# Kernel tuning notes

Hardware: AMD Instinct MI355X
Metric: run time of the kernel (lower is better)

Reference implementation:

```python
import jax, jax.numpy as jnp
import numpy as np

N_GENE = 50000
N_PROT = 50000
E = 500000
D = 128          # embedding_dim
C = 32           # out_channels = embedding_dim // attn_heads
F_IN = 256       # in_channels per node type
NUM_MP = 3       # metapaths: [gene-gene, gene-protein, protein-protein]


def _glorot(key, shape):
    lim = float(np.sqrt(6.0 / (shape[0] + shape[1])))
    return jax.random.uniform(key, shape, minval=-lim, maxval=lim, dtype=jnp.float32)


def setup_inputs() -> dict:
    key = jax.random.key(0)
    ks = jax.random.split(key, 24)
    inp = {
        "x_gene": jax.random.normal(ks[0], (N_GENE, F_IN), dtype=jnp.float32),
        "x_protein": jax.random.normal(ks[1], (N_PROT, F_IN), dtype=jnp.float32),
        # node-type projections linear_l / linear_r
        "Wl_gene": _glorot(ks[2], (D, F_IN)), "bl_gene": jnp.zeros((D,), jnp.float32),
        "Wr_gene": _glorot(ks[3], (D, F_IN)), "br_gene": jnp.zeros((D,), jnp.float32),
        "Wl_prot": _glorot(ks[4], (D, F_IN)), "bl_prot": jnp.zeros((D,), jnp.float32),
        "Wr_prot": _glorot(ks[5], (D, F_IN)), "br_prot": jnp.zeros((D,), jnp.float32),
        # per-metapath attention params (stacked over 3 metapaths)
        "alW": jnp.stack([_glorot(ks[6 + i], (C, D)) for i in range(NUM_MP)]),
        "alb": jnp.zeros((NUM_MP, C), jnp.float32),
        "arW": jnp.stack([_glorot(ks[9 + i], (C, D)) for i in range(NUM_MP)]),
        "arb": jnp.zeros((NUM_MP, C), jnp.float32),
        "qw": jnp.stack([_glorot(ks[12 + i], (2 * C, 1)) for i in range(NUM_MP)]),
        "sharp": jnp.ones((NUM_MP,), jnp.float32),  # 'sharpening' alpha_activation
        # per-node-type relation-weighting conv (Linear(D, 1))
        "conv_gene_W": _glorot(ks[15], (1, D)), "conv_gene_b": jnp.zeros((1,), jnp.float32),
        "conv_prot_W": _glorot(ks[16], (1, D)), "conv_prot_b": jnp.zeros((1,), jnp.float32),
        # edge indices: row 0 = head node (aggregation target), row 1 = tail node
        "edge_gg": jax.random.randint(ks[17], (2, E), 0, N_GENE, dtype=jnp.int32),
        "edge_gp": jnp.stack([jax.random.randint(ks[18], (E,), 0, N_GENE, dtype=jnp.int32),
                               jax.random.randint(ks[19], (E,), 0, N_PROT, dtype=jnp.int32)]),
        "edge_pp": jax.random.randint(ks[20], (2, E), 0, N_PROT, dtype=jnp.int32),
    }
    return inp


def _segment_softmax(scores, seg, n):
    # numerically stable softmax over variable-size neighborhoods (grouped by seg)
    m = jax.ops.segment_max(scores, seg, num_segments=n)
    m = jnp.where(jnp.isfinite(m), m, 0.0)
    ex = jnp.exp(scores - m[seg])
    denom = jax.ops.segment_sum(ex, seg, num_segments=n)
    return ex / (denom[seg] + 1e-16)


def _metapath_agg(l_head, r_tail, alW, alb, arW, arb, qw, sharp, eidx, n_head):
    # alpha_l / alpha_r node-level projections [N, C]
    al = l_head @ alW.T + alb
    ar = r_tail @ arW.T + arb
    src, dst = eidx[0], eidx[1]           # head (aggregate-at), tail (message-from)
    a_i = al[src]                          # [E, C]
    a_j = ar[dst]                          # [E, C]
    # attn_q: Tanh then Linear(2C -> 1, no bias); 'sharpening' scales the logit
    e = (jnp.tanh(jnp.concatenate([a_i, a_j], axis=1)) @ qw)[:, 0] * sharp  # [E]
    alpha = _segment_softmax(e, src, n_head)
    # message x_j * alpha, scatter-add into head nodes (aggr='add')
    return jax.ops.segment_sum(r_tail[dst] * alpha[:, None], src, num_segments=n_head)


def _relation_combine(aggs, l_self, conv_W, conv_b):
    # stack relation embeddings + self embedding: [N, R, D]
    out = jnp.stack(aggs + [l_self], axis=1)
    beta = jax.nn.softmax(out @ conv_W.T + conv_b, axis=1)  # [N, R, 1]
    return jax.nn.relu(jnp.sum(out * beta, axis=1))          # [N, D]


def reference(x_gene, x_protein, Wl_gene, bl_gene, Wr_gene, br_gene,
              Wl_prot, bl_prot, Wr_prot, br_prot,
              alW, alb, arW, arb, qw, sharp,
              conv_gene_W, conv_gene_b, conv_prot_W, conv_prot_b,
              edge_gg, edge_gp, edge_pp):
    # first layer: l/r projections from raw features
    l_gene = x_gene @ Wl_gene.T + bl_gene
    r_gene = x_gene @ Wr_gene.T + br_gene
    l_prot = x_protein @ Wl_prot.T + bl_prot
    r_prot = x_protein @ Wr_prot.T + br_prot

    # metapath 0: gene <- gene ; metapath 1: gene <- protein ; metapath 2: protein <- protein
    agg_gg = _metapath_agg(l_gene, r_gene, alW[0], alb[0], arW[0], arb[0], qw[0], sharp[0], edge_gg, N_GENE)
    agg_gp = _metapath_agg(l_gene, r_prot, alW[1], alb[1], arW[1], arb[1], qw[1], sharp[1], edge_gp, N_GENE)
    agg_pp = _metapath_agg(l_prot, r_prot, alW[2], alb[2], arW[2], arb[2], qw[2], sharp[2], edge_pp, N_PROT)

    out_gene = _relation_combine([agg_gg, agg_gp], l_gene, conv_gene_W, conv_gene_b)
    out_prot = _relation_combine([agg_pp], l_prot, conv_prot_W, conv_prot_b)
    return (out_gene, out_prot)
```

## Files before the change

kernel.cpp:

```cpp
#include <hip/hip_runtime.h>
#include <hip/hip_bf16.h>


typedef __attribute__((ext_vector_type(8))) short short8;
typedef __attribute__((ext_vector_type(4))) float floatx4;

__device__ __forceinline__ void gload16(const void* g, void* l) {
  __builtin_amdgcn_global_load_lds(
      (const __attribute__((address_space(1))) void*)g,
      (__attribute__((address_space(3))) void*)l, 16, 0, 0);
}

__device__ __forceinline__ ushort f2b(float x) {
  __hip_bfloat16 h = __float2bfloat16(x);
  return *reinterpret_cast<ushort*>(&h);
}
__device__ __forceinline__ float b2f_lo(unsigned v) { return __uint_as_float(v << 16); }
__device__ __forceinline__ float b2f_hi(unsigned v) { return __uint_as_float(v & 0xffff0000u); }

struct CvtArgs {
  const float* src[8];
  ushort* dst[8];
  int valid[8];
  int total[8];
  int bstart[9];
};
__global__ __launch_bounds__(256) void cvt_multi(CvtArgs a) {
  int b = blockIdx.x;
  int e = 0;
#pragma unroll
  for (int j = 1; j < 8; ++j)
    if (b >= a.bstart[j]) e = j;
  int i = ((b - a.bstart[e]) * 256 + threadIdx.x) * 4;
  if (i >= a.total[e]) return;
  float4 v = make_float4(0.f, 0.f, 0.f, 0.f);
  if (i < a.valid[e]) v = *(const float4*)(a.src[e] + i);
  ushort4 o;
  o.x = f2b(v.x); o.y = f2b(v.y); o.z = f2b(v.z); o.w = f2b(v.w);
  *(ushort4*)(a.dst[e] + i) = o;
}

struct ProjArgs {
  const ushort* xb[2];
  const ushort* Wb[2];
  const float* bl[2];
  const float* br[2];
  ushort* lb[2];
  ushort* rb[2];
  int N[2];
};
__global__ __launch_bounds__(256) void proj_lr_mfma(ProjArgs g) {
  const int ty = blockIdx.z;
  const ushort* xb = g.xb[ty];
  __shared__ ushort As[128 * 32];
  __shared__ ushort Bs[128 * 32];
  const int tid = threadIdx.x;
  const int lane = tid & 63;
  const int wave = tid >> 6;
  const int wm = wave & 1, wn = wave >> 1;
  const int rowBase = blockIdx.x * 128;
  const int colHalf = blockIdx.y;
  const ushort* Wbase = g.Wb[ty] + (size_t)colHalf * 128 * 256;

  floatx4 acc[4][4] = {};

  const int srow = tid >> 2, schk = tid & 3;
  for (int k0 = 0; k0 < 256; k0 += 32) {
#pragma unroll
    for (int i = 0; i < 2; ++i) {
      gload16(xb + (size_t)(rowBase + srow + i * 64) * 256 + k0 + schk * 8,
              &As[(tid + i * 256) * 8]);
      gload16(Wbase + (size_t)(srow + i * 64) * 256 + k0 + schk * 8,
              &Bs[(tid + i * 256) * 8]);
    }
    __syncthreads();
    short8 bf[4];
#pragma unroll
    for (int nt = 0; nt < 4; ++nt)
      bf[nt] = *(const short8*)&Bs[(wn * 64 + nt * 16 + (lane & 15)) * 32 + (lane >> 4) * 8];
#pragma unroll
    for (int mt = 0; mt < 4; ++mt) {
      short8 a = *(const short8*)&As[(wm * 64 + mt * 16 + (lane & 15)) * 32 + (lane >> 4) * 8];
#pragma unroll
      for (int nt = 0; nt < 4; ++nt)
        acc[mt][nt] = __builtin_amdgcn_mfma_f32_16x16x32_bf16(a, bf[nt], acc[mt][nt], 0, 0, 0);
    }
    __syncthreads();
  }

  const int N = g.N[ty];
  const float* bias = colHalf ? g.br[ty] : g.bl[ty];
  ushort* outp = colHalf ? g.rb[ty] : g.lb[ty];
#pragma unroll
  for (int mt = 0; mt < 4; ++mt)
#pragma unroll
    for (int nt = 0; nt < 4; ++nt) {
      int col = wn * 64 + nt * 16 + (lane & 15);
      float bv = bias[col];
#pragma unroll
      for (int vi = 0; vi < 4; ++vi) {
        int row = rowBase + wm * 64 + mt * 16 + (lane >> 4) * 4 + vi;
        if (row < N) outp[(size_t)row * 128 + col] = f2b(acc[mt][nt][vi] + bv);
      }
    }
}

struct AttnArgs {
  const ushort* Ab[4];
  const ushort* Wb[4];
  const float* bias[4];
  const float* q0[4];
  const float* q1[4];
  float* o0[4];
  float* o1[4];
  int N[4];
  int BN[4];
};
__global__ __launch_bounds__(256) void attn_proj_multi(AttnArgs g) {
  const int ei = blockIdx.y;
  const ushort* Ab = g.Ab[ei];
  const ushort* Wb = g.Wb[ei];
  const int N = g.N[ei], BN = g.BN[ei];
  const int NB = BN >> 4;
  __shared__ ushort As[128 * 32];
  __shared__ ushort Ws[64 * 128];
  const int tid = threadIdx.x;
  const int lane = tid & 63;
  const int wave = tid >> 6;
  const int rowBase = blockIdx.x * 128;

  for (int i = 0; i < NB; ++i) {
    int idx = tid + i * 256;
    gload16(Wb + (size_t)idx * 8, &Ws[idx * 8]);
  }

  floatx4 acc[2][4] = {};
  for (int k0 = 0; k0 < 128; k0 += 32) {
#pragma unroll
    for (int i = 0; i < 2; ++i) {
      int t = tid + i * 256;
      gload16(Ab + (size_t)(rowBase + (t >> 2)) * 128 + k0 + (t & 3) * 8, &As[t * 8]);
    }
    __syncthreads();
    short8 bf[4];
#pragma unroll
    for (int nt = 0; nt < 4; ++nt)
      if (nt < NB)
        bf[nt] = *(const short8*)&Ws[(nt * 16 + (lane & 15)) * 128 + k0 + (lane >> 4) * 8];
#pragma unroll
    for (int mt = 0; mt < 2; ++mt) {
      short8 a = *(const short8*)&As[(wave * 32 + mt * 16 + (lane & 15)) * 32 + (lane >> 4) * 8];
#pragma unroll
      for (int nt = 0; nt < 4; ++nt)
        if (nt < NB)
          acc[mt][nt] = __builtin_amdgcn_mfma_f32_16x16x32_bf16(a, bf[nt], acc[mt][nt], 0, 0, 0);
    }
    __syncthreads();
  }

  const float* bias = g.bias[ei];
  const int l15 = lane & 15;
  const bool two = (NB == 4);
  float bv[4];
#pragma unroll
  for (int nt = 0; nt < 4; ++nt) bv[nt] = (nt < NB) ? bias[nt * 16 + l15] : 0.f;
  float q0v0 = g.q0[ei][l15], q0v1 = g.q0[ei][16 + l15];
  float q1v0 = 0.f, q1v1 = 0.f;
  if (two) { q1v0 = g.q1[ei][l15]; q1v1 = g.q1[ei][16 + l15]; }
  float* o0 = g.o0[ei];
  float* o1 = g.o1[ei];
#pragma unroll
  for (int mt = 0; mt < 2; ++mt)
#pragma unroll
    for (int vi = 0; vi < 4; ++vi) {
      float slo = tanhf(acc[mt][0][vi] + bv[0]) * q0v0
                + tanhf(acc[mt][1][vi] + bv[1]) * q0v1;
      float shi = 0.f;
      if (two)
        shi = tanhf(acc[mt][2][vi] + bv[2]) * q1v0
            + tanhf(acc[mt][3][vi] + bv[3]) * q1v1;
#pragma unroll
      for (int m = 8; m >= 1; m >>= 1) {
        slo += __shfl_xor(slo, m, 64);
        shi += __shfl_xor(shi, m, 64);
      }
      const int row = rowBase + wave * 32 + mt * 16 + (lane >> 4) * 4 + vi;
      if (l15 == 0 && row < N) {
        o0[row] = slo;
        if (two) o1[row] = shi;
      }
    }
}

__global__ __launch_bounds__(256) void hist3_kernel(
    const int* __restrict__ e0, const int* __restrict__ e1,
    const int* __restrict__ e2, int* __restrict__ deg,
    int* __restrict__ rank, int E, int NG) {
  int e = blockIdx.x * 256 + threadIdx.x;
  if (e >= 3 * E) return;
  int mp = (e >= 2 * E) ? 2 : ((e >= E) ? 1 : 0);
  int el = e - mp * E;
  const int* ep = (mp == 0) ? e0 : (mp == 1) ? e1 : e2;
  int segb = (mp == 2) ? 2 * NG : mp * NG;
  rank[e] = atomicAdd(&deg[segb + ep[el]], 1);
}

__global__ __launch_bounds__(256) void scanA_kernel(
    const int* __restrict__ deg, int* __restrict__ offsets,
    int* __restrict__ tile_tot, int n) {
  __shared__ int wtot[4];
  const int t = threadIdx.x;
  const int base = blockIdx.x * 2048 + t * 8;
  int v[8], pre[8], s = 0;
#pragma unroll
  for (int j = 0; j < 8; ++j) {
    v[j] = (base + j < n) ? deg[base + j] : 0;
    pre[j] = s;
    s += v[j];
  }
  const int lane = t & 63, wv = t >> 6;
  int x = s;
#pragma unroll
  for (int o = 1; o < 64; o <<= 1) {
    int u = __shfl_up(x, o, 64);
    if (lane >= o) x += u;
  }
  if (lane == 63) wtot[wv] = x;
  __syncthreads();
  int wpre = 0;
#pragma unroll
  for (int j = 0; j < 4; ++j) wpre += (j < wv) ? wtot[j] : 0;
  int excl = wpre + x - s;
#pragma unroll
  for (int j = 0; j < 8; ++j)
    if (base + j < n) offsets[base + j] = excl + pre[j];
  if (t == 255) tile_tot[blockIdx.x] = wpre + x;
}

__global__ __launch_bounds__(256) void scanB_kernel(
    const int* __restrict__ tile_tot, int* __restrict__ tile_pre,
    int* __restrict__ offsets, int T, int n) {
  __shared__ int wtot[4];
  const int t = threadIdx.x;
  int v = (t < T) ? tile_tot[t] : 0;
  const int lane = t & 63, wv = t >> 6;
  int x = v;
#pragma unroll
  for (int o = 1; o < 64; o <<= 1) {
    int u = __shfl_up(x, o, 64);
    if (lane >= o) x += u;
  }
  if (lane == 63) wtot[wv] = x;
  __syncthreads();
  int wpre = 0;
#pragma unroll
  for (int j = 0; j < 4; ++j) wpre += (j < wv) ? wtot[j] : 0;
  if (t < T) tile_pre[t] = wpre + x - v;
  if (t == 255) offsets[n] = wpre + x;
}

__global__ __launch_bounds__(256) void scanC_kernel(
    int* __restrict__ offsets, const int* __restrict__ tile_pre, int n) {
  const int add = tile_pre[blockIdx.x];
  const int base = blockIdx.x * 2048 + threadIdx.x * 8;
#pragma unroll
  for (int j = 0; j < 8; ++j)
    if (base + j < n) offsets[base + j] += add;
}

__global__ __launch_bounds__(256) void scatter3_kernel(
    const int* __restrict__ e0, const int* __restrict__ e1,
    const int* __restrict__ e2, const int* __restrict__ rank,
    const int* __restrict__ offsets,
    const float* __restrict__ tl3, const float* __restrict__ tr3,
    const float* __restrict__ sharp, int2* __restrict__ recs,
    int E, int NG, int NP) {
  int e = blockIdx.x * 256 + threadIdx.x;
  if (e >= 3 * E) return;
  int mp = (e >= 2 * E) ? 2 : ((e >= E) ? 1 : 0);
  int el = e - mp * E;
  const int* ep = (mp == 0) ? e0 : (mp == 1) ? e1 : e2;
  int s = ep[el], d = ep[el + E];
  int hb = (mp == 2) ? 2 * NG : mp * NG;
  int tb = (mp == 0) ? 0 : (mp == 1) ? NG : NG + NP;
  float w = expf((tl3[hb + s] + tr3[tb + d]) * sharp[mp]);
  recs[offsets[hb + s] + rank[e]] = make_int2(d << 8, __float_as_int(w));
}

__global__ __launch_bounds__(256) void gather_combine(
    const ushort* __restrict__ rb_gene, const ushort* __restrict__ rb_prot,
    const ushort* __restrict__ lb_gene, const ushort* __restrict__ lb_prot,
    const int* __restrict__ offsets, const int2* __restrict__ recs,
    const float* __restrict__ cgW, const float* __restrict__ cgb,
    const float* __restrict__ cpW, const float* __restrict__ cpb,
    float* __restrict__ out_gene, float* __restrict__ out_prot,
    int NG, int NP) {
  const int lane = threadIdx.x & 63;
  const int l16 = lane & 15;
  const int node = blockIdx.x * 16 + (threadIdx.x >> 4);
  if (node >= NG + NP) return;
  const bool isGene = node < NG;
  const unsigned coloff = (unsigned)l16 << 4;
  const unsigned OMASK = 0x00FFFF00u;

  const int h0 = isGene ? node : NG + node;
  const int j0a = offsets[h0];
  const int ca = offsets[h0 + 1] - j0a;
  int j0b = 0, cb2 = 0;
  if (isGene) {
    j0b = offsets[NG + node];
    cb2 = offsets[NG + node + 1] - j0b;
  }

  float a0[8] = {0.f, 0.f, 0.f, 0.f, 0.f, 0.f, 0.f, 0.f};
  float a1[8] = {0.f, 0.f, 0.f, 0.f, 0.f, 0.f, 0.f, 0.f};
  float ds0 = 0.f, ds1 = 0.f;
  const ushort* rtA = isGene ? rb_gene : rb_prot;

  if (isGene) {
    const int cmax = (ca > cb2) ? ca : cb2;
    if (cmax > 0) {
      int2 rA0 = recs[j0a];
      int2 rA1 = recs[j0a + ((1 < ca) ? 1 : 0)];
      int2 rB0 = recs[j0b];
      int2 rB1 = recs[j0b + ((1 < cb2) ? 1 : 0)];
      const int nit = (cmax + 1) >> 1;
      for (int it = 0; it < nit; ++it) {
        const int b = it * 2;
        const float wA0 = (b < ca)      ? __int_as_float(rA0.y) : 0.f;
        const float wA1 = (b + 1 < ca)  ? __int_as_float(rA1.y) : 0.f;
        const float wB0 = (b < cb2)     ? __int_as_float(rB0.y) : 0.f;
        const float wB1 = (b + 1 < cb2) ? __int_as_float(rB1.y) : 0.f;
        const uint4 vA0 = *(const uint4*)((const char*)rtA + (((unsigned)rA0.x & OMASK) + coloff));
        const uint4 vA1 = *(const uint4*)((const char*)rtA + (((unsigned)rA1.x & OMASK) + coloff));
        const uint4 vB0 = *(const uint4*)((const char*)rb_prot + (((unsigned)rB0.x & OMASK) + coloff));
        const uint4 vB1 = *(const uint4*)((const char*)rb_prot + (((unsigned)rB1.x & OMASK) + coloff));
        const int nb = b + 2;
        rA0 = recs[j0a + ((nb < ca) ? nb : 0)];
        rA1 = recs[j0a + ((nb + 1 < ca) ? nb + 1 : 0)];
        rB0 = recs[j0b + ((nb < cb2) ? nb : 0)];
        rB1 = recs[j0b + ((nb + 1 < cb2) ? nb + 1 : 0)];
        ds0 += wA0 + wA1;
        a0[0] += b2f_lo(vA0.x) * wA0 + b2f_lo(vA1.x) * wA1;
        a0[1] += b2f_hi(vA0.x) * wA0 + b2f_hi(vA1.x) * wA1;
        a0[2] += b2f_lo(vA0.y) * wA0 + b2f_lo(vA1.y) * wA1;
        a0[3] += b2f_hi(vA0.y) * wA0 + b2f_hi(vA1.y) * wA1;
        a0[4] += b2f_lo(vA0.z) * wA0 + b2f_lo(vA1.z) * wA1;
        a0[5] += b2f_hi(vA0.z) * wA0 + b2f_hi(vA1.z) * wA1;
        a0[6] += b2f_lo(vA0.w) * wA0 + b2f_lo(vA1.w) * wA1;
        a0[7] += b2f_hi(vA0.w) * wA0 + b2f_hi(vA1.w) * wA1;
        ds1 += wB0 + wB1;
        a1[0] += b2f_lo(vB0.x) * wB0 + b2f_lo(vB1.x) * wB1;
        a1[1] += b2f_hi(vB0.x) * wB0 + b2f_hi(vB1.x) * wB1;
        a1[2] += b2f_lo(vB0.y) * wB0 + b2f_lo(vB1.y) * wB1;
        a1[3] += b2f_hi(vB0.y) * wB0 + b2f_hi(vB1.y) * wB1;
        a1[4] += b2f_lo(vB0.z) * wB0 + b2f_lo(vB1.z) * wB1;
        a1[5] += b2f_hi(vB0.z) * wB0 + b2f_hi(vB1.z) * wB1;
        a1[6] += b2f_lo(vB0.w) * wB0 + b2f_lo(vB1.w) * wB1;
        a1[7] += b2f_hi(vB0.w) * wB0 + b2f_hi(vB1.w) * wB1;
      }
    }
  } else {
    if (ca > 0) {
      int2 r0 = recs[j0a];
      int2 r1 = recs[j0a + ((1 < ca) ? 1 : 0)];
      int2 r2 = recs[j0a + ((2 < ca) ? 2 : 0)];
      int2 r3 = recs[j0a + ((3 < ca) ? 3 : 0)];
      const int nit = (ca + 3) >> 2;
      for (int it = 0; it < nit; ++it) {
        const int b = it * 4;
        const float w0 = (b < ca)     ? __int_as_float(r0.y) : 0.f;
        const float w1 = (b + 1 < ca) ? __int_as_float(r1.y) : 0.f;
        const float w2 = (b + 2 < ca) ? __int_as_float(r2.y) : 0.f;
        const float w3 = (b + 3 < ca) ? __int_as_float(r3.y) : 0.f;
        const uint4 v0 = *(const uint4*)((const char*)rtA + (((unsigned)r0.x & OMASK) + coloff));
        const uint4 v1 = *(const uint4*)((const char*)rtA + (((unsigned)r1.x & OMASK) + coloff));
        const uint4 v2 = *(const uint4*)((const char*)rtA + (((unsigned)r2.x & OMASK) + coloff));
        const uint4 v3 = *(const uint4*)((const char*)rtA + (((unsigned)r3.x & OMASK) + coloff));
        const int nb = b + 4;
        r0 = recs[j0a + ((nb < ca) ? nb : 0)];
        r1 = recs[j0a + ((nb + 1 < ca) ? nb + 1 : 0)];
        r2 = recs[j0a + ((nb + 2 < ca) ? nb + 2 : 0)];
        r3 = recs[j0a + ((nb + 3 < ca) ? nb + 3 : 0)];
        ds0 += (w0 + w1) + (w2 + w3);
        a0[0] += b2f_lo(v0.x) * w0 + b2f_lo(v1.x) * w1 + b2f_lo(v2.x) * w2 + b2f_lo(v3.x) * w3;
        a0[1] += b2f_hi(v0.x) * w0 + b2f_hi(v1.x) * w1 + b2f_hi(v2.x) * w2 + b2f_hi(v3.x) * w3;
        a0[2] += b2f_lo(v0.y) * w0 + b2f_lo(v1.y) * w1 + b2f_lo(v2.y) * w2 + b2f_lo(v3.y) * w3;
        a0[3] += b2f_hi(v0.y) * w0 + b2f_hi(v1.y) * w1 + b2f_hi(v2.y) * w2 + b2f_hi(v3.y) * w3;
        a0[4] += b2f_lo(v0.z) * w0 + b2f_lo(v1.z) * w1 + b2f_lo(v2.z) * w2 + b2f_lo(v3.z) * w3;
        a0[5] += b2f_hi(v0.z) * w0 + b2f_hi(v1.z) * w1 + b2f_hi(v2.z) * w2 + b2f_hi(v3.z) * w3;
        a0[6] += b2f_lo(v0.w) * w0 + b2f_lo(v1.w) * w1 + b2f_lo(v2.w) * w2 + b2f_lo(v3.w) * w3;
        a0[7] += b2f_hi(v0.w) * w0 + b2f_hi(v1.w) * w1 + b2f_hi(v2.w) * w2 + b2f_hi(v3.w) * w3;
      }
    }
  }

  const float inv0 = 1.f / (ds0 + 1e-16f);
  const float inv1 = 1.f / (ds1 + 1e-16f);
  float g0[8], g1[8], self[8];
#pragma unroll
  for (int c = 0; c < 8; ++c) { g0[c] = a0[c] * inv0; g1[c] = a1[c] * inv1; }
  {
    const ushort* lbp = isGene ? lb_gene + (size_t)node * 128
                               : lb_prot + (size_t)(node - NG) * 128;
    uint4 sv = *(const uint4*)(lbp + l16 * 8);
    self[0] = b2f_lo(sv.x); self[1] = b2f_hi(sv.x);
    self[2] = b2f_lo(sv.y); self[3] = b2f_hi(sv.y);
    self[4] = b2f_lo(sv.z); self[5] = b2f_hi(sv.z);
    self[6] = b2f_lo(sv.w); self[7] = b2f_hi(sv.w);
  }

  const float* cW = isGene ? cgW : cpW;
  const float cb = isGene ? cgb[0] : cpb[0];
  const float4 wlo = *(const float4*)(cW + l16 * 8);
  const float4 whi = *(const float4*)(cW + l16 * 8 + 4);
  float p0 = g0[0] * wlo.x + g0[1] * wlo.y + g0[2] * wlo.z + g0[3] * wlo.w +
             g0[4] * whi.x + g0[5] * whi.y + g0[6] * whi.z + g0[7] * whi.w;
  float p1 = g1[0] * wlo.x + g1[1] * wlo.y + g1[2] * wlo.z + g1[3] * wlo.w +
             g1[4] * whi.x + g1[5] * whi.y + g1[6] * whi.z + g1[7] * whi.w;
  float ps = self[0] * wlo.x + self[1] * wlo.y + self[2] * wlo.z + self[3] * wlo.w +
             self[4] * whi.x + self[5] * whi.y + self[6] * whi.z + self[7] * whi.w;
#pragma unroll
  for (int m = 8; m >= 1; m >>= 1) {
    p0 += __shfl_xor(p0, m, 64);
    p1 += __shfl_xor(p1, m, 64);
    ps += __shfl_xor(ps, m, 64);
  }
  const float s0 = p0 + cb, s1 = p1 + cb, ss = ps + cb;
  const float mx = isGene ? fmaxf(fmaxf(s0, s1), ss) : fmaxf(s0, ss);
  const float e0 = expf(s0 - mx);
  const float e1 = isGene ? expf(s1 - mx) : 0.f;
  const float es = expf(ss - mx);
  const float sum = e0 + e1 + es;
  const float b0 = e0 / sum, b1 = e1 / sum, bs = es / sum;

  float4 o0, o1;
  o0.x = fmaxf(g0[0] * b0 + g1[0] * b1 + self[0] * bs, 0.f);
  o0.y = fmaxf(g0[1] * b0 + g1[1] * b1 + self[1] * bs, 0.f);
  o0.z = fmaxf(g0[2] * b0 + g1[2] * b1 + self[2] * bs, 0.f);
  o0.w = fmaxf(g0[3] * b0 + g1[3] * b1 + self[3] * bs, 0.f);
  o1.x = fmaxf(g0[4] * b0 + g1[4] * b1 + self[4] * bs, 0.f);
  o1.y = fmaxf(g0[5] * b0 + g1[5] * b1 + self[5] * bs, 0.f);
  o1.z = fmaxf(g0[6] * b0 + g1[6] * b1 + self[6] * bs, 0.f);
  o1.w = fmaxf(g0[7] * b0 + g1[7] * b1 + self[7] * bs, 0.f);
  float* op = isGene ? out_gene + (size_t)node * 128
                     : out_prot + (size_t)(node - NG) * 128;
  *(float4*)(op + l16 * 8) = o0;
  *(float4*)(op + l16 * 8 + 4) = o1;
}

extern "C" void kernel_launch(void* const* d_in, const int* in_sizes, int n_in,
                              void* d_out, int out_size, void* d_ws,
                              size_t ws_size, hipStream_t stream) {
  const float* x_gene  = (const float*)d_in[0];
  const float* x_prot  = (const float*)d_in[1];
  const float* Wl_gene = (const float*)d_in[2];
  const float* bl_gene = (const float*)d_in[3];
  const float* Wr_gene = (const float*)d_in[4];
  const float* br_gene = (const float*)d_in[5];
  const float* Wl_prot = (const float*)d_in[6];
  const float* bl_prot = (const float*)d_in[7];
  const float* Wr_prot = (const float*)d_in[8];
  const float* br_prot = (const float*)d_in[9];
  const float* alW     = (const float*)d_in[10];
  const float* alb     = (const float*)d_in[11];
  const float* arW     = (const float*)d_in[12];
  const float* arb     = (const float*)d_in[13];
  const float* qw      = (const float*)d_in[14];
  const float* sharp   = (const float*)d_in[15];
  const float* cgW     = (const float*)d_in[16];
  const float* cgb     = (const float*)d_in[17];
  const float* cpW     = (const float*)d_in[18];
  const float* cpb     = (const float*)d_in[19];
  const int* e_gg      = (const int*)d_in[20];
  const int* e_gp      = (const int*)d_in[21];
  const int* e_pp      = (const int*)d_in[22];

  const int NG = in_sizes[0] / 256;
  const int NP = in_sizes[1] / 256;
  const int E  = in_sizes[20] / 2;
  const int NPG = (NG + 127) & ~127;
  const int NPP = (NP + 127) & ~127;
  const int NT = 2 * NG + NP;
  const int NR = NG + 2 * NP;

  char* base = (char*)d_ws;
  size_t off = 0;
  auto alloc = [&](size_t bytes) {
    void* p = base + off;
    off = (off + bytes + 255) & ~(size_t)255;
    return p;
  };
  ushort* xb_gene = (ushort*)alloc((size_t)NPG * 256 * 2);
  ushort* xb_prot = (ushort*)alloc((size_t)NPP * 256 * 2);

  ushort* Wlr_gene = (ushort*)alloc(256 * 256 * 2);
  ushort* Wlr_prot = (ushort*)alloc(256 * 256 * 2);
  ushort* alWb     = (ushort*)alloc(96 * 128 * 2);
  ushort* arWb     = (ushort*)alloc(96 * 128 * 2);
  ushort* lb_gene  = (ushort*)alloc((size_t)NPG * 128 * 2);
  ushort* rb_gene  = (ushort*)alloc((size_t)NPG * 128 * 2);
  ushort* lb_prot  = (ushort*)alloc((size_t)NPP * 128 * 2);
  ushort* rb_prot  = (ushort*)alloc((size_t)NPP * 128 * 2);
  int*    deg      = (int*)alloc((size_t)NT * 4);
  int*    offsets  = (int*)alloc((size_t)(NT + 1) * 4);
  const int TILES  = (NT + 2047) / 2048;
  int*    tile_tot = (int*)alloc((size_t)TILES * 4);
  int*    tile_pre = (int*)alloc((size_t)TILES * 4);
  int*    rank     = (int*)alloc((size_t)(3 * E) * 4);
  int2*   recs     = (int2*)alloc((size_t)(3 * E) * sizeof(int2));
  float*  tl3      = (float*)alloc((size_t)NT * 4);
  float*  tr3      = (float*)alloc((size_t)NR * 4);

  float* out_gene = (float*)d_out;
  float* out_prot = out_gene + (size_t)NG * 128;

  dim3 blk(256);

  {
    CvtArgs a;
    const float* srcs[8] = {x_gene, x_prot, Wl_gene, Wr_gene, Wl_prot, Wr_prot, alW, arW};
    ushort* dsts[8] = {xb_gene, xb_prot, Wlr_gene, Wlr_gene + 128 * 256,
                       Wlr_prot, Wlr_prot + 128 * 256, alWb, arWb};
    int valids[8] = {NG * 256, NP * 256, 128 * 256, 128 * 256, 128 * 256, 128 * 256, 96 * 128, 96 * 128};
    int totals[8] = {NPG * 256, NPP * 256, 128 * 256, 128 * 256, 128 * 256, 128 * 256, 96 * 128, 96 * 128};
    int b = 0;
    for (int j = 0; j < 8; ++j) {
      a.src[j] = srcs[j]; a.dst[j] = dsts[j];
      a.valid[j] = valids[j]; a.total[j] = totals[j];
      a.bstart[j] = b;
      b += (totals[j] / 4 + 255) / 256;
    }
    a.bstart[8] = b;
    cvt_multi<<<b, blk, 0, stream>>>(a);
  }

  {
    ProjArgs p;
    p.xb[0] = xb_gene; p.xb[1] = xb_prot;
    p.Wb[0] = Wlr_gene; p.Wb[1] = Wlr_prot;
    p.bl[0] = bl_gene; p.bl[1] = bl_prot;
    p.br[0] = br_gene; p.br[1] = br_prot;
    p.lb[0] = lb_gene; p.lb[1] = lb_prot;
    p.rb[0] = rb_gene; p.rb[1] = rb_prot;
    p.N[0] = NG; p.N[1] = NP;
    proj_lr_mfma<<<dim3(NPG / 128, 2, 2), blk, 0, stream>>>(p);
  }

  {
    AttnArgs a;
    a.Ab[0] = lb_gene; a.Wb[0] = alWb;            a.bias[0] = alb;      a.N[0] = NG; a.BN[0] = 64;
    a.q0[0] = qw + 0;  a.q1[0] = qw + 64;  a.o0[0] = tl3;          a.o1[0] = tl3 + NG;
    a.Ab[1] = rb_gene; a.Wb[1] = arWb;            a.bias[1] = arb;      a.N[1] = NG; a.BN[1] = 32;
    a.q0[1] = qw + 32; a.q1[1] = qw + 32;  a.o0[1] = tr3;          a.o1[1] = tr3;
    a.Ab[2] = lb_prot; a.Wb[2] = alWb + 64 * 128; a.bias[2] = alb + 64; a.N[2] = NP; a.BN[2] = 32;
    a.q0[2] = qw + 128; a.q1[2] = qw + 128; a.o0[2] = tl3 + 2 * NG; a.o1[2] = tl3 + 2 * NG;
    a.Ab[3] = rb_prot; a.Wb[3] = arWb + 32 * 128; a.bias[3] = arb + 32; a.N[3] = NP; a.BN[3] = 64;
    a.q0[3] = qw + 96; a.q1[3] = qw + 160; a.o0[3] = tr3 + NG;     a.o1[3] = tr3 + NG + NP;
    attn_proj_multi<<<dim3(NPG / 128, 4), blk, 0, stream>>>(a);
  }

  const int gridE3 = (3 * E + 255) / 256;
  hipMemsetAsync(deg, 0, (size_t)NT * sizeof(int), stream);
  hist3_kernel<<<gridE3, blk, 0, stream>>>(e_gg, e_gp, e_pp, deg, rank, E, NG);
  scanA_kernel<<<TILES, blk, 0, stream>>>(deg, offsets, tile_tot, NT);
  scanB_kernel<<<1, blk, 0, stream>>>(tile_tot, tile_pre, offsets, TILES, NT);
  scanC_kernel<<<TILES, blk, 0, stream>>>(offsets, tile_pre, NT);
  scatter3_kernel<<<gridE3, blk, 0, stream>>>(e_gg, e_gp, e_pp, rank, offsets,
                                              tl3, tr3, sharp, recs, E, NG, NP);

  gather_combine<<<(NG + NP + 15) / 16, blk, 0, stream>>>(
      rb_gene, rb_prot, lb_gene, lb_prot, offsets, recs,
      cgW, cgb, cpW, cpb, out_gene, out_prot, NG, NP);
}
```

Before: 429.8 us.

## Fuse fp32-to-bf16 feature conversion into projection GEMM and widen gather unroll

The projection kernel now reads fp32 node features directly and converts them to bf16 while staging into shared memory. This removes the separate conversion pass and its bf16 copy of x, which was a full extra read and write of both feature matrices. Each block now has 512 threads and computes both the l and r outputs (256 columns), so x is read once instead of twice. Separately, the gene aggregation loop is unrolled from 2 to 4 edges per iteration to keep more gathers in flight, at the cost of more registers.

```diff
diff --git a/kernel.cpp b/kernel.cpp
--- a/kernel.cpp
+++ b/kernel.cpp
@@ -41,7 +41,7 @@
 }
 
 struct ProjArgs {
-  const ushort* xb[2];
+  const float* x[2];
   const ushort* Wb[2];
   const float* bl[2];
   const float* br[2];
@@ -49,30 +49,38 @@
   ushort* rb[2];
   int N[2];
 };
-__global__ __launch_bounds__(256) void proj_lr_mfma(ProjArgs g) {
-  const int ty = blockIdx.z;
-  const ushort* xb = g.xb[ty];
+__global__ __launch_bounds__(512) void proj_lr_mfma(ProjArgs g) {
+  const int ty = blockIdx.y;
+  const float* xp = g.x[ty];
+  const int N = g.N[ty];
   __shared__ ushort As[128 * 32];
-  __shared__ ushort Bs[128 * 32];
+  __shared__ ushort Bs[256 * 32];
   const int tid = threadIdx.x;
   const int lane = tid & 63;
   const int wave = tid >> 6;
   const int wm = wave & 1, wn = wave >> 1;
   const int rowBase = blockIdx.x * 128;
-  const int colHalf = blockIdx.y;
-  const ushort* Wbase = g.Wb[ty] + (size_t)colHalf * 128 * 256;
+  const ushort* Wb = g.Wb[ty];
 
   floatx4 acc[4][4] = {};
 
-  const int srow = tid >> 2, schk = tid & 3;
+  const int arow = tid >> 2, achk = tid & 3;
+  const int xrow = min(rowBase + arow, N - 1);
+  const float* xrp = xp + (size_t)xrow * 256;
+
   for (int k0 = 0; k0 < 256; k0 += 32) {
 #pragma unroll
     for (int i = 0; i < 2; ++i) {
-      gload16(xb + (size_t)(rowBase + srow + i * 64) * 256 + k0 + schk * 8,
-              &As[(tid + i * 256) * 8]);
-      gload16(Wbase + (size_t)(srow + i * 64) * 256 + k0 + schk * 8,
-              &Bs[(tid + i * 256) * 8]);
-    }
+      int t = tid + i * 512;
+      gload16(Wb + (size_t)(t >> 2) * 256 + k0 + (t & 3) * 8, &Bs[t * 8]);
+    }
+    float4 lo = *(const float4*)(xrp + k0 + achk * 8);
+    float4 hi = *(const float4*)(xrp + k0 + achk * 8 + 4);
+    ushort4 c0, c1;
+    c0.x = f2b(lo.x); c0.y = f2b(lo.y); c0.z = f2b(lo.z); c0.w = f2b(lo.w);
+    c1.x = f2b(hi.x); c1.y = f2b(hi.y); c1.z = f2b(hi.z); c1.w = f2b(hi.w);
+    *(ushort4*)&As[arow * 32 + achk * 8] = c0;
+    *(ushort4*)&As[arow * 32 + achk * 8 + 4] = c1;
     __syncthreads();
     short8 bf[4];
 #pragma unroll
@@ -88,19 +96,18 @@
     __syncthreads();
   }
 
-  const int N = g.N[ty];
-  const float* bias = colHalf ? g.br[ty] : g.bl[ty];
-  ushort* outp = colHalf ? g.rb[ty] : g.lb[ty];
 #pragma unroll
   for (int mt = 0; mt < 4; ++mt)
 #pragma unroll
     for (int nt = 0; nt < 4; ++nt) {
-      int col = wn * 64 + nt * 16 + (lane & 15);
-      float bv = bias[col];
+      const int col = wn * 64 + nt * 16 + (lane & 15);
+      const int half = col >> 7, c = col & 127;
+      const float bv = (half ? g.br[ty] : g.bl[ty])[c];
+      ushort* outp = half ? g.rb[ty] : g.lb[ty];
 #pragma unroll
       for (int vi = 0; vi < 4; ++vi) {
         int row = rowBase + wm * 64 + mt * 16 + (lane >> 4) * 4 + vi;
-        if (row < N) outp[(size_t)row * 128 + col] = f2b(acc[mt][nt][vi] + bv);
+        if (row < N) outp[(size_t)row * 128 + c] = f2b(acc[mt][nt][vi] + bv);
       }
     }
 }
@@ -320,44 +327,43 @@
   if (isGene) {
     const int cmax = (ca > cb2) ? ca : cb2;
     if (cmax > 0) {
-      int2 rA0 = recs[j0a];
-      int2 rA1 = recs[j0a + ((1 < ca) ? 1 : 0)];
-      int2 rB0 = recs[j0b];
-      int2 rB1 = recs[j0b + ((1 < cb2) ? 1 : 0)];
-      const int nit = (cmax + 1) >> 1;
+      int2 rA[4], rB[4];
+#pragma unroll
+      for (int p = 0; p < 4; ++p) {
+        rA[p] = recs[j0a + ((p < ca) ? p : 0)];
+        rB[p] = recs[j0b + ((p < cb2) ? p : 0)];
+      }
+      const int nit = (cmax + 3) >> 2;
       for (int it = 0; it < nit; ++it) {
-        const int b = it * 2;
-        const float wA0 = (b < ca)      ? __int_as_float(rA0.y) : 0.f;
-        const float wA1 = (b + 1 < ca)  ? __int_as_float(rA1.y) : 0.f;
-        const float wB0 = (b < cb2)     ? __int_as_float(rB0.y) : 0.f;
-        const float wB1 = (b + 1 < cb2) ? __int_as_float(rB1.y) : 0.f;
-        const uint4 vA0 = *(const uint4*)((const char*)rtA + (((unsigned)rA0.x & OMASK) + coloff));
-        const uint4 vA1 = *(const uint4*)((const char*)rtA + (((unsigned)rA1.x & OMASK) + coloff));
-        const uint4 vB0 = *(const uint4*)((const char*)rb_prot + (((unsigned)rB0.x & OMASK) + coloff));
-        const uint4 vB1 = *(const uint4*)((const char*)rb_prot + (((unsigned)rB1.x & OMASK) + coloff));
-        const int nb = b + 2;
-        rA0 = recs[j0a + ((nb < ca) ? nb : 0)];
-        rA1 = recs[j0a + ((nb + 1 < ca) ? nb + 1 : 0)];
-        rB0 = recs[j0b + ((nb < cb2) ? nb : 0)];
-        rB1 = recs[j0b + ((nb + 1 < cb2) ? nb + 1 : 0)];
-        ds0 += wA0 + wA1;
-        a0[0] += b2f_lo(vA0.x) * wA0 + b2f_lo(vA1.x) * wA1;
-        a0[1] += b2f_hi(vA0.x) * wA0 + b2f_hi(vA1.x) * wA1;
-        a0[2] += b2f_lo(vA0.y) * wA0 + b2f_lo(vA1.y) * wA1;
-        a0[3] += b2f_hi(vA0.y) * wA0 + b2f_hi(vA1.y) * wA1;
-        a0[4] += b2f_lo(vA0.z) * wA0 + b2f_lo(vA1.z) * wA1;
-        a0[5] += b2f_hi(vA0.z) * wA0 + b2f_hi(vA1.z) * wA1;
-        a0[6] += b2f_lo(vA0.w) * wA0 + b2f_lo(vA1.w) * wA1;
-        a0[7] += b2f_hi(vA0.w) * wA0 + b2f_hi(vA1.w) * wA1;
-        ds1 += wB0 + wB1;
-        a1[0] += b2f_lo(vB0.x) * wB0 + b2f_lo(vB1.x) * wB1;
-        a1[1] += b2f_hi(vB0.x) * wB0 + b2f_hi(vB1.x) * wB1;
-        a1[2] += b2f_lo(vB0.y) * wB0 + b2f_lo(vB1.y) * wB1;
-        a1[3] += b2f_hi(vB0.y) * wB0 + b2f_hi(vB1.y) * wB1;
-        a1[4] += b2f_lo(vB0.z) * wB0 + b2f_lo(vB1.z) * wB1;
-        a1[5] += b2f_hi(vB0.z) * wB0 + b2f_hi(vB1.z) * wB1;
-        a1[6] += b2f_lo(vB0.w) * wB0 + b2f_lo(vB1.w) * wB1;
-        a1[7] += b2f_hi(vB0.w) * wB0 + b2f_hi(vB1.w) * wB1;
+        const int b = it * 4;
+        float wA[4], wB[4];
+        uint4 vA[4], vB[4];
+#pragma unroll
+        for (int p = 0; p < 4; ++p) {
+          wA[p] = (b + p < ca)  ? __int_as_float(rA[p].y) : 0.f;
+          wB[p] = (b + p < cb2) ? __int_as_float(rB[p].y) : 0.f;
+          vA[p] = *(const uint4*)((const char*)rtA + (((unsigned)rA[p].x & OMASK) + coloff));
+          vB[p] = *(const uint4*)((const char*)rb_prot + (((unsigned)rB[p].x & OMASK) + coloff));
+        }
+        const int nb = b + 4;
+#pragma unroll
+        for (int p = 0; p < 4; ++p) {
+          rA[p] = recs[j0a + ((nb + p < ca) ? nb + p : 0)];
+          rB[p] = recs[j0b + ((nb + p < cb2) ? nb + p : 0)];
+        }
+#pragma unroll
+        for (int p = 0; p < 4; ++p) {
+          ds0 += wA[p];
+          a0[0] += b2f_lo(vA[p].x) * wA[p]; a0[1] += b2f_hi(vA[p].x) * wA[p];
+          a0[2] += b2f_lo(vA[p].y) * wA[p]; a0[3] += b2f_hi(vA[p].y) * wA[p];
+          a0[4] += b2f_lo(vA[p].z) * wA[p]; a0[5] += b2f_hi(vA[p].z) * wA[p];
+          a0[6] += b2f_lo(vA[p].w) * wA[p]; a0[7] += b2f_hi(vA[p].w) * wA[p];
+          ds1 += wB[p];
+          a1[0] += b2f_lo(vB[p].x) * wB[p]; a1[1] += b2f_hi(vB[p].x) * wB[p];
+          a1[2] += b2f_lo(vB[p].y) * wB[p]; a1[3] += b2f_hi(vB[p].y) * wB[p];
+          a1[4] += b2f_lo(vB[p].z) * wB[p]; a1[5] += b2f_hi(vB[p].z) * wB[p];
+          a1[6] += b2f_lo(vB[p].w) * wB[p]; a1[7] += b2f_hi(vB[p].w) * wB[p];
+        }
       }
     }
   } else {
@@ -480,7 +486,6 @@
   const int NP = in_sizes[1] / 256;
   const int E  = in_sizes[20] / 2;
   const int NPG = (NG + 127) & ~127;
-  const int NPP = (NP + 127) & ~127;
   const int NT = 2 * NG + NP;
   const int NR = NG + 2 * NP;
 
@@ -491,17 +496,14 @@
     off = (off + bytes + 255) & ~(size_t)255;
     return p;
   };
-  ushort* xb_gene = (ushort*)alloc((size_t)NPG * 256 * 2);
-  ushort* xb_prot = (ushort*)alloc((size_t)NPP * 256 * 2);
-
   ushort* Wlr_gene = (ushort*)alloc(256 * 256 * 2);
   ushort* Wlr_prot = (ushort*)alloc(256 * 256 * 2);
   ushort* alWb     = (ushort*)alloc(96 * 128 * 2);
   ushort* arWb     = (ushort*)alloc(96 * 128 * 2);
   ushort* lb_gene  = (ushort*)alloc((size_t)NPG * 128 * 2);
   ushort* rb_gene  = (ushort*)alloc((size_t)NPG * 128 * 2);
-  ushort* lb_prot  = (ushort*)alloc((size_t)NPP * 128 * 2);
-  ushort* rb_prot  = (ushort*)alloc((size_t)NPP * 128 * 2);
+  ushort* lb_prot  = (ushort*)alloc((size_t)NPG * 128 * 2);
+  ushort* rb_prot  = (ushort*)alloc((size_t)NPG * 128 * 2);
   int*    deg      = (int*)alloc((size_t)NT * 4);
   int*    offsets  = (int*)alloc((size_t)(NT + 1) * 4);
   const int TILES  = (NT + 2047) / 2048;
@@ -519,17 +521,19 @@
 
   {
     CvtArgs a;
-    const float* srcs[8] = {x_gene, x_prot, Wl_gene, Wr_gene, Wl_prot, Wr_prot, alW, arW};
-    ushort* dsts[8] = {xb_gene, xb_prot, Wlr_gene, Wlr_gene + 128 * 256,
-                       Wlr_prot, Wlr_prot + 128 * 256, alWb, arWb};
-    int valids[8] = {NG * 256, NP * 256, 128 * 256, 128 * 256, 128 * 256, 128 * 256, 96 * 128, 96 * 128};
-    int totals[8] = {NPG * 256, NPP * 256, 128 * 256, 128 * 256, 128 * 256, 128 * 256, 96 * 128, 96 * 128};
+    const float* srcs[8] = {Wl_gene, Wr_gene, Wl_prot, Wr_prot, alW, arW,
+                            Wl_gene, Wl_gene};
+    ushort* dsts[8] = {Wlr_gene, Wlr_gene + 128 * 256,
+                       Wlr_prot, Wlr_prot + 128 * 256, alWb, arWb,
+                       Wlr_gene, Wlr_gene};
+    int sizes[8] = {128 * 256, 128 * 256, 128 * 256, 128 * 256,
+                    96 * 128, 96 * 128, 0, 0};
     int b = 0;
     for (int j = 0; j < 8; ++j) {
       a.src[j] = srcs[j]; a.dst[j] = dsts[j];
-      a.valid[j] = valids[j]; a.total[j] = totals[j];
+      a.valid[j] = sizes[j]; a.total[j] = sizes[j];
       a.bstart[j] = b;
-      b += (totals[j] / 4 + 255) / 256;
+      b += (sizes[j] / 4 + 255) / 256;
     }
     a.bstart[8] = b;
     cvt_multi<<<b, blk, 0, stream>>>(a);
@@ -537,14 +541,14 @@
 
   {
     ProjArgs p;
-    p.xb[0] = xb_gene; p.xb[1] = xb_prot;
+    p.x[0] = x_gene; p.x[1] = x_prot;
     p.Wb[0] = Wlr_gene; p.Wb[1] = Wlr_prot;
     p.bl[0] = bl_gene; p.bl[1] = bl_prot;
     p.br[0] = br_gene; p.br[1] = br_prot;
     p.lb[0] = lb_gene; p.lb[1] = lb_prot;
     p.rb[0] = rb_gene; p.rb[1] = rb_prot;
     p.N[0] = NG; p.N[1] = NP;
-    proj_lr_mfma<<<dim3(NPG / 128, 2, 2), blk, 0, stream>>>(p);
+    proj_lr_mfma<<<dim3(NPG / 128, 2), dim3(512), 0, stream>>>(p);
   }
 
   {
```

Measured after the change: 407.9 us. -5.1%, faster.
